# Performance work log

Hardware: AMD Instinct MI355X
Metric: run time of the kernel (lower is better)

The kernel has to match this reference:

```python
import jax, jax.numpy as jnp
import numpy as np

X0, Y0 = -51.2, -51.2          # cfg.X_RANGE[0], cfg.Y_RANGE[0]
VOXEL = 0.2                    # cfg.VOXEL_SIZE
GRID_W, GRID_H = 512, 512      # cfg.GRID_W, cfg.GRID_H
EPS = 1e-5                     # BatchNorm eps
B, N, C_IN = 2, 250000, 5
C_OUT2 = 128                   # out_channels * 2


def setup_inputs() -> dict:
    key = jax.random.key(0)
    ks = jax.random.split(key, 12)
    # points: x,y in a box slightly larger than the BEV range so mask is exercised
    xy = jax.random.uniform(ks[0], (B, N, 2), minval=-55.0, maxval=55.0, dtype=jnp.float32)
    z = jax.random.uniform(ks[1], (B, N, 1), minval=-3.0, maxval=1.0, dtype=jnp.float32)
    it = jax.random.uniform(ks[2], (B, N, 2), dtype=jnp.float32)  # intensity, time
    points = jnp.concatenate([xy, z, it], axis=-1)

    def lin_w(k, fi, fo):
        return jax.random.normal(k, (fi, fo), dtype=jnp.float32) / np.float32(np.sqrt(fi))

    return {
        "points": points,
        "W1": lin_w(ks[3], C_IN + 3, 64), "b1": jnp.zeros((64,), jnp.float32),
        "g1": jnp.ones((64,), jnp.float32), "be1": jnp.zeros((64,), jnp.float32),
        "m1": 0.1 * jax.random.normal(ks[4], (64,), jnp.float32),
        "v1": jnp.ones((64,), jnp.float32) + 0.1 * jax.random.uniform(ks[5], (64,)),
        "W2": lin_w(ks[6], 64, 64), "b2": jnp.zeros((64,), jnp.float32),
        "g2": jnp.ones((64,), jnp.float32), "be2": jnp.zeros((64,), jnp.float32),
        "m2": 0.1 * jax.random.normal(ks[7], (64,), jnp.float32),
        "v2": jnp.ones((64,), jnp.float32) + 0.1 * jax.random.uniform(ks[8], (64,)),
        "W3": lin_w(ks[9], 64, C_OUT2), "b3": jnp.zeros((C_OUT2,), jnp.float32),
    }


def _bn(x, g, be, m, v):
    # eval-mode BatchNorm1d: per-channel affine normalize
    return (x - m) * jax.lax.rsqrt(v + EPS) * g + be


def _frame(pts, W1, b1, g1, be1, m1, v1, W2, b2, g2, be2, m2, v2, W3, b3):
    # pts: [N, 5]
    # torch .long() truncates toward zero; astype(int32) does the same
    x_idx = ((pts[:, 0] - X0) / VOXEL).astype(jnp.int32)
    y_idx = ((pts[:, 1] - Y0) / VOXEL).astype(jnp.int32)
    mask = (x_idx >= 0) & (x_idx < GRID_W) & (y_idx >= 0) & (y_idx < GRID_H)

    xc = x_idx.astype(pts.dtype) * VOXEL + (X0 + VOXEL / 2)
    yc = y_idx.astype(pts.dtype) * VOXEL + (Y0 + VOXEL / 2)
    # z_center == pts[:,2], so the third residual is exactly zero (faithful)
    pts_aug = jnp.concatenate(
        [pts,
         (pts[:, 0] - xc)[:, None],
         (pts[:, 1] - yc)[:, None],
         jnp.zeros_like(pts[:, 2])[:, None]], axis=1)  # [N, 8]

    h = jax.nn.relu(_bn(pts_aug @ W1 + b1, g1, be1, m1, v1))
    h = jax.nn.relu(_bn(h @ W2 + b2, g2, be2, m2, v2))
    feat = h @ W3 + b3  # [N, 128]

    n_cells = GRID_H * GRID_W
    # invalid points routed to dummy segment n_cells
    idx = jnp.where(mask, y_idx * GRID_W + x_idx, n_cells)
    last = jax.ops.segment_max(jnp.arange(N, dtype=jnp.int32), idx,
                               num_segments=n_cells + 1)[:n_cells]  # [HW]
    canvas = jnp.where(last[:, None] >= 0,
                       feat[jnp.maximum(last, 0)], 0.0)  # [HW, 128]
    return canvas.T.reshape(C_OUT2, GRID_H, GRID_W)


def reference(points, W1, b1, g1, be1, m1, v1, W2, b2, g2, be2, m2, v2, W3, b3):
    f = lambda pts: _frame(pts, W1, b1, g1, be1, m1, v1,
                           W2, b2, g2, be2, m2, v2, W3, b3)
    return jax.vmap(f)(points)  # [B, 128, GRID_H, GRID_W]
```

## Files before the change

kernel.cpp:

```cpp
#include <hip/hip_runtime.h>

typedef __attribute__((ext_vector_type(8))) __bf16 bf16x8;
typedef __attribute__((ext_vector_type(4))) float f32x4;

#define GRID_W 512
#define GRID_H 512
#define HW (GRID_W * GRID_H)
#define NPTS 250000
#define NB 2
#define NCELLS (NB * HW)
#define SCAT_BLOCKS ((NB * NPTS + 255) / 256)

__device__ __forceinline__ void cell_of(float x, float y, int& xi, int& yi) {
    xi = (int)__fmul_rn(__fadd_rn(x, 51.2f), 5.0f);
    yi = (int)__fmul_rn(__fadd_rn(y, 51.2f), 5.0f);
}

__global__ __launch_bounds__(256) void k_scat_prep(
    const float* __restrict__ pts, int* __restrict__ win,
    const float* __restrict__ W1, const float* __restrict__ b1,
    const float* __restrict__ g1, const float* __restrict__ be1,
    const float* __restrict__ m1, const float* __restrict__ v1,
    const float* __restrict__ W2, const float* __restrict__ b2,
    const float* __restrict__ g2, const float* __restrict__ be2,
    const float* __restrict__ m2, const float* __restrict__ v2,
    const float* __restrict__ W3, const float* __restrict__ b3,
    float* __restrict__ w1f, float* __restrict__ bb1,
    float* __restrict__ bb2, float* __restrict__ b3f,
    __bf16* __restrict__ w2hi, __bf16* __restrict__ w2lo,
    __bf16* __restrict__ w3hi, __bf16* __restrict__ w3lo)
{
    if (blockIdx.x < SCAT_BLOCKS) {
        int gid = blockIdx.x * 256 + threadIdx.x;
        if (gid >= NB * NPTS) return;
        int b = gid / NPTS;
        int i = gid - b * NPTS;
        const float* p = pts + (size_t)gid * 5;
        int xi, yi;
        cell_of(p[0], p[1], xi, yi);
        if (xi >= 0 && xi < GRID_W && yi >= 0 && yi < GRID_H) {
            atomicMax(&win[b * HW + yi * GRID_W + xi], i);
        }
        return;
    }
    int gid = (blockIdx.x - SCAT_BLOCKS) * 256 + threadIdx.x;
    if (gid < 64) {
        int t = gid;
        float s1 = g1[t] / sqrtf(v1[t] + 1e-5f);
        bb1[t] = (b1[t] - m1[t]) * s1 + be1[t];
        float s2 = g2[t] / sqrtf(v2[t] + 1e-5f);
        bb2[t] = (b2[t] - m2[t]) * s2 + be2[t];
    } else if (gid < 192) {
        b3f[gid - 64] = b3[gid - 64];
    } else if (gid < 704) {
        int e = gid - 192;
        int j = e & 63;
        float s1 = g1[j] / sqrtf(v1[j] + 1e-5f);
        w1f[e] = W1[e] * s1;
    } else if (gid < 4800) {
        int e = gid - 704;
        int j = e & 7, n = (e >> 3) & 15, g = (e >> 7) & 7, nt = e >> 10;
        int k = g * 8 + j, ng = nt * 16 + n;
        float s2 = g2[ng] / sqrtf(v2[ng] + 1e-5f);
        float wf = W2[k * 64 + ng] * s2;
        __bf16 hi = (__bf16)wf;
        w2hi[e] = hi;
        w2lo[e] = (__bf16)(wf - (float)hi);
    } else if (gid < 12992) {
        int e = gid - 4800;
        int j = e & 7, n = (e >> 3) & 15, g = (e >> 7) & 7, nt = e >> 10;
        int k = g * 8 + j, ng = nt * 16 + n;
        float wf = W3[k * 128 + ng];
        __bf16 hi = (__bf16)wf;
        w3hi[e] = hi;
        w3lo[e] = (__bf16)(wf - (float)hi);
    }
}

__global__ __launch_bounds__(256, 4) void k_mlp(
    const float* __restrict__ pts, const int* __restrict__ win,
    const float* __restrict__ w1f, const float* __restrict__ bb1,
    const float* __restrict__ bb2, const float* __restrict__ b3f,
    const __bf16* __restrict__ w2hi, const __bf16* __restrict__ w2lo,
    const __bf16* __restrict__ w3hi, const __bf16* __restrict__ w3lo,
    float* __restrict__ out)
{
    __shared__ float sW1f[512];
    __shared__ float sBB1[64], sBB2[64], sB3[128];
    __shared__ __bf16 sAhi[4][4096];

    const int t = threadIdx.x;
    const int wv = t >> 6;
    const int lane = t & 63;

    const int bI = blockIdx.x >> 10;
    const int cellBase = (blockIdx.x & 1023) * 256;
    const int gcell = bI * HW + cellBase + t;

    int w = win[gcell];
    unsigned long long mb = __ballot(w >= 0);

    float px = 0.f, py = 0.f, pz = 0.f, pin = 0.f, ptm = 0.f;
    if (w >= 0) {
        const float* p = pts + ((size_t)bI * NPTS + w) * 5;
        px = p[0]; py = p[1]; pz = p[2]; pin = p[3]; ptm = p[4];
    }

    if (t < 128)      ((float4*)sW1f)[t]       = ((const float4*)w1f)[t];
    else if (t < 144) ((float4*)sBB1)[t - 128] = ((const float4*)bb1)[t - 128];
    else if (t < 160) ((float4*)sBB2)[t - 144] = ((const float4*)bb2)[t - 144];
    else if (t < 192) ((float4*)sB3)[t - 160]  = ((const float4*)b3f)[t - 160];
    __syncthreads();

    float a8[8];
    a8[0] = px; a8[1] = py; a8[2] = pz; a8[3] = pin; a8[4] = ptm;
    {
        int xi, yi;
        cell_of(px, py, xi, yi);
        float xc = __fadd_rn(__fmul_rn((float)xi, 0.2f), -51.1f);
        float yc = __fadd_rn(__fmul_rn((float)yi, 0.2f), -51.1f);
        a8[5] = __fadd_rn(px, -xc);
        a8[6] = __fadd_rn(py, -yc);
        a8[7] = 0.0f;
    }
    float h1[64];
#pragma unroll
    for (int j4 = 0; j4 < 16; ++j4) {
        float4 acc = ((const float4*)sBB1)[j4];
#pragma unroll
        for (int k = 0; k < 8; ++k) {
            float4 wq = ((const float4*)sW1f)[k * 16 + j4];
            acc.x = fmaf(a8[k], wq.x, acc.x);
            acc.y = fmaf(a8[k], wq.y, acc.y);
            acc.z = fmaf(a8[k], wq.z, acc.z);
            acc.w = fmaf(a8[k], wq.w, acc.w);
        }
        h1[j4 * 4 + 0] = fmaxf(acc.x, 0.0f);
        h1[j4 * 4 + 1] = fmaxf(acc.y, 0.0f);
        h1[j4 * 4 + 2] = fmaxf(acc.z, 0.0f);
        h1[j4 * 4 + 3] = fmaxf(acc.w, 0.0f);
    }

    {
        int abase = (lane >> 4) * 1024 + (lane & 15) * 8;
#pragma unroll
        for (int g = 0; g < 8; ++g) {
            bf16x8 hi8;
#pragma unroll
            for (int j = 0; j < 8; ++j)
                hi8[j] = (__bf16)h1[g * 8 + j];
            *(bf16x8*)&sAhi[wv][abase + g * 128] = hi8;
        }
    }

    bf16x8 Ahi[4][2];
#pragma unroll
    for (int mt = 0; mt < 4; ++mt)
#pragma unroll
        for (int ks = 0; ks < 2; ++ks)
            Ahi[mt][ks] = *(const bf16x8*)&sAhi[wv][mt * 1024 + ks * 512 + lane * 8];

#pragma unroll
    for (int nt = 0; nt < 4; ++nt) {
        bf16x8 Bhi[2], Blo[2];
#pragma unroll
        for (int ks = 0; ks < 2; ++ks) {
            int off = nt * 1024 + ks * 512 + lane * 8;
            Bhi[ks] = *(const bf16x8*)&w2hi[off];
            Blo[ks] = *(const bf16x8*)&w2lo[off];
        }
        f32x4 zero = {0.f, 0.f, 0.f, 0.f};
        f32x4 acc[4] = {zero, zero, zero, zero};
#pragma unroll
        for (int mt = 0; mt < 4; ++mt)
#pragma unroll
            for (int ks = 0; ks < 2; ++ks) {
                acc[mt] = __builtin_amdgcn_mfma_f32_16x16x32_bf16(Ahi[mt][ks], Bhi[ks], acc[mt], 0, 0, 0);
                acc[mt] = __builtin_amdgcn_mfma_f32_16x16x32_bf16(Ahi[mt][ks], Blo[ks], acc[mt], 0, 0, 0);
            }
        float bb2l = sBB2[nt * 16 + (lane & 15)];
        int gg = nt * 2 + ((lane & 15) >> 3);
        int jj = lane & 7;
#pragma unroll
        for (int mt = 0; mt < 4; ++mt)
#pragma unroll
            for (int r = 0; r < 4; ++r) {
                float h = fmaxf(acc[mt][r] + bb2l, 0.0f);
                int off = mt * 1024 + gg * 128 + ((lane >> 4) * 4 + r) * 8 + jj;
                sAhi[wv][off] = (__bf16)h;
            }
    }

#pragma unroll
    for (int mt = 0; mt < 4; ++mt)
#pragma unroll
        for (int ks = 0; ks < 2; ++ks)
            Ahi[mt][ks] = *(const bf16x8*)&sAhi[wv][mt * 1024 + ks * 512 + lane * 8];

    float4 mk[4];
#pragma unroll
    for (int mt = 0; mt < 4; ++mt) {
        int base = mt * 16 + (lane >> 4) * 4;
        mk[mt].x = ((mb >> (base + 0)) & 1ull) ? 1.0f : 0.0f;
        mk[mt].y = ((mb >> (base + 1)) & 1ull) ? 1.0f : 0.0f;
        mk[mt].z = ((mb >> (base + 2)) & 1ull) ? 1.0f : 0.0f;
        mk[mt].w = ((mb >> (base + 3)) & 1ull) ? 1.0f : 0.0f;
    }

    float* sTw = (float*)sAhi[wv];
    float* outW = out + (size_t)bI * 128 * HW + cellBase + wv * 64;
    const int g = lane >> 4;
    const int ch = lane & 15;
#pragma unroll
    for (int nt = 0; nt < 8; ++nt) {
        bf16x8 Bhi[2], Blo[2];
#pragma unroll
        for (int ks = 0; ks < 2; ++ks) {
            int off = nt * 1024 + ks * 512 + lane * 8;
            Bhi[ks] = *(const bf16x8*)&w3hi[off];
            Blo[ks] = *(const bf16x8*)&w3lo[off];
        }
        f32x4 zero = {0.f, 0.f, 0.f, 0.f};
        f32x4 acc[4] = {zero, zero, zero, zero};
#pragma unroll
        for (int mt = 0; mt < 4; ++mt)
#pragma unroll
            for (int ks = 0; ks < 2; ++ks) {
                acc[mt] = __builtin_amdgcn_mfma_f32_16x16x32_bf16(Ahi[mt][ks], Bhi[ks], acc[mt], 0, 0, 0);
                acc[mt] = __builtin_amdgcn_mfma_f32_16x16x32_bf16(Ahi[mt][ks], Blo[ks], acc[mt], 0, 0, 0);
            }
        float b3l = sB3[nt * 16 + ch];

#pragma unroll
        for (int mt = 0; mt < 4; ++mt) {
            f32x4 o;
            o[0] = (acc[mt][0] + b3l) * mk[mt].x;
            o[1] = (acc[mt][1] + b3l) * mk[mt].y;
            o[2] = (acc[mt][2] + b3l) * mk[mt].z;
            o[3] = (acc[mt][3] + b3l) * mk[mt].w;
            *(f32x4*)&sTw[ch * 68 + mt * 16 + g * 4] = o;
        }
#pragma unroll
        for (int j = 0; j < 4; ++j) {
            int chl = j * 4 + g;
            f32x4 v = *(const f32x4*)&sTw[chl * 68 + ch * 4];
            *(f32x4*)(outW + (size_t)(nt * 16 + chl) * HW + ch * 4) = v;
        }
    }
}

extern "C" void kernel_launch(void* const* d_in, const int* in_sizes, int n_in,
                              void* d_out, int out_size, void* d_ws, size_t ws_size,
                              hipStream_t stream) {
    const float* pts = (const float*)d_in[0];
    const float* W1  = (const float*)d_in[1];
    const float* b1  = (const float*)d_in[2];
    const float* g1  = (const float*)d_in[3];
    const float* be1 = (const float*)d_in[4];
    const float* m1  = (const float*)d_in[5];
    const float* v1  = (const float*)d_in[6];
    const float* W2  = (const float*)d_in[7];
    const float* b2  = (const float*)d_in[8];
    const float* g2  = (const float*)d_in[9];
    const float* be2 = (const float*)d_in[10];
    const float* m2  = (const float*)d_in[11];
    const float* v2  = (const float*)d_in[12];
    const float* W3  = (const float*)d_in[13];
    const float* b3  = (const float*)d_in[14];
    float* out = (float*)d_out;

    char* wsb = (char*)d_ws;
    int*    win  = (int*)wsb;
    float*  w1f  = (float*)(wsb + 2097152);
    float*  bb1  = (float*)(wsb + 2097152 + 2048);
    float*  bb2  = (float*)(wsb + 2097152 + 2304);
    float*  b3f  = (float*)(wsb + 2097152 + 2560);
    __bf16* w2hi = (__bf16*)(wsb + 2097152 + 3072);
    __bf16* w2lo = w2hi + 4096;
    __bf16* w3hi = w2lo + 4096;
    __bf16* w3lo = w3hi + 8192;

    hipMemsetAsync(win, 0xFF, (size_t)NCELLS * sizeof(int), stream);
    k_scat_prep<<<SCAT_BLOCKS + 51, 256, 0, stream>>>(pts, win,
        W1, b1, g1, be1, m1, v1,
        W2, b2, g2, be2, m2, v2, W3, b3,
        w1f, bb1, bb2, b3f, w2hi, w2lo, w3hi, w3lo);
    k_mlp<<<NCELLS / 256, 256, 0, stream>>>(pts, win,
        w1f, bb1, bb2, b3f, w2hi, w2lo, w3hi, w3lo, out);
}
```

Baseline: 83.43 us.

## Share output transpose staging across waves for full-row coalesced canvas stores

Output staging moves from a per-wave 16x64 tile to a block-wide 16x256 shared tile. Each wave now writes whole 1KB contiguous channel rows to global memory instead of 256-byte segments. This targets store efficiency on the large canvas write that dominates traffic. In exchange it adds block-wide barriers twice per channel tile, which serialise the waves, and the scalar LDS stores may introduce bank conflicts.

```diff
diff --git a/kernel.cpp b/kernel.cpp
--- a/kernel.cpp
+++ b/kernel.cpp
@@ -14,6 +14,11 @@
 __device__ __forceinline__ void cell_of(float x, float y, int& xi, int& yi) {
     xi = (int)__fmul_rn(__fadd_rn(x, 51.2f), 5.0f);
     yi = (int)__fmul_rn(__fadd_rn(y, 51.2f), 5.0f);
+}
+
+__device__ __forceinline__ void lds_barrier() {
+    asm volatile("s_waitcnt lgkmcnt(0)" ::: "memory");
+    __builtin_amdgcn_s_barrier();
 }
 
 __global__ __launch_bounds__(256) void k_scat_prep(
@@ -197,6 +202,8 @@
         for (int ks = 0; ks < 2; ++ks)
             Ahi[mt][ks] = *(const bf16x8*)&sAhi[wv][mt * 1024 + ks * 512 + lane * 8];
 
+    lds_barrier();
+
     float4 mk[4];
 #pragma unroll
     for (int mt = 0; mt < 4; ++mt) {
@@ -207,8 +214,8 @@
         mk[mt].w = ((mb >> (base + 3)) & 1ull) ? 1.0f : 0.0f;
     }
 
-    float* sTw = (float*)sAhi[wv];
-    float* outW = out + (size_t)bI * 128 * HW + cellBase + wv * 64;
+    float* sOut = (float*)sAhi;
+    float* outBat = out + (size_t)bI * 128 * HW + cellBase;
     const int g = lane >> 4;
     const int ch = lane & 15;
 #pragma unroll
@@ -231,21 +238,25 @@
             }
         float b3l = sB3[nt * 16 + ch];
 
-#pragma unroll
-        for (int mt = 0; mt < 4; ++mt) {
-            f32x4 o;
-            o[0] = (acc[mt][0] + b3l) * mk[mt].x;
-            o[1] = (acc[mt][1] + b3l) * mk[mt].y;
-            o[2] = (acc[mt][2] + b3l) * mk[mt].z;
-            o[3] = (acc[mt][3] + b3l) * mk[mt].w;
-            *(f32x4*)&sTw[ch * 68 + mt * 16 + g * 4] = o;
-        }
+        {
+            int cb = wv * 64 + g * 4;
+#pragma unroll
+            for (int mt = 0; mt < 4; ++mt) {
+                float* so = &sOut[ch * 260 + cb + mt * 16];
+                so[0] = (acc[mt][0] + b3l) * mk[mt].x;
+                so[1] = (acc[mt][1] + b3l) * mk[mt].y;
+                so[2] = (acc[mt][2] + b3l) * mk[mt].z;
+                so[3] = (acc[mt][3] + b3l) * mk[mt].w;
+            }
+        }
+        lds_barrier();
 #pragma unroll
         for (int j = 0; j < 4; ++j) {
-            int chl = j * 4 + g;
-            f32x4 v = *(const f32x4*)&sTw[chl * 68 + ch * 4];
-            *(f32x4*)(outW + (size_t)(nt * 16 + chl) * HW + ch * 4) = v;
-        }
+            int chl = wv * 4 + j;
+            f32x4 v = *(const f32x4*)&sOut[chl * 260 + lane * 4];
+            *(f32x4*)(outBat + (size_t)(nt * 16 + chl) * HW + lane * 4) = v;
+        }
+        lds_barrier();
     }
 }
 
```

Measured after the change: 89.31 us. 1.07x slower.
